# Optimization experiments

Measured on AMD Instinct MI355X. Metric: run time of the kernel, lower is better.

The kernel has to match this reference:

```python
import jax, jax.numpy as jnp
import numpy as np

N_LAYERS = 3
D = 32          # in = hidden = out channels (hardcoded in module)
N = 100_000     # nodes
E = 3_200_000   # edges (avg degree 32)
EPS = 1e-5
SLOPE = 0.01    # LeakyReLU default negative slope


def setup_inputs() -> dict:
    key = jax.random.key(0)
    ks = jax.random.split(key, 12)
    x = jax.random.normal(ks[0], (N, D), jnp.float32)
    edge_index = jax.random.randint(ks[1], (2, E), 0, N)
    edge_attr = jax.random.normal(ks[2], (E, 1), jnp.float32)  # unused by the conv
    s = 1.0 / np.sqrt(D)  # torch Linear default init range
    W = lambda k: jax.random.uniform(k, (N_LAYERS, D, D), jnp.float32, -s, s)
    b = lambda k: jax.random.uniform(k, (N_LAYERS, D), jnp.float32, -s, s)
    return dict(
        patch_embs=x, edge_index=edge_index, edge_attr=edge_attr,
        Wk=W(ks[3]), bk=b(ks[4]),   # lin_key   (applied to x_i / target)
        Wq=W(ks[5]), bq=b(ks[6]),   # lin_query (applied to x_j / source)
        Wv=W(ks[7]), bv=b(ks[8]),   # lin_value (applied to x_j / source)
        Ws=W(ks[9]), bs=b(ks[10]),  # lin_skip  (applied to x_i)
        gamma=jnp.ones((N_LAYERS, D), jnp.float32),
        beta=jnp.zeros((N_LAYERS, D), jnp.float32),
    )


def _res_gated_conv(x, Wk, bk, Wq, bq, Wv, bv, Ws, bs, src, dst):
    # Project per-node first (cheap), gather per-edge after.
    k = x @ Wk.T + bk   # [N,D] key   of target
    q = x @ Wq.T + bq   # [N,D] query of source
    v = x @ Wv.T + bv   # [N,D] value of source
    eta = jax.nn.sigmoid(k[dst] + q[src])          # [E,D] gate
    agg = jax.ops.segment_sum(eta * v[src], dst, num_segments=x.shape[0])
    return agg + (x @ Ws.T + bs)


def _batchnorm(x, g, b):
    mu = x.mean(axis=0)
    var = x.var(axis=0)  # biased, as in torch BN training forward
    return (x - mu) * jax.lax.rsqrt(var + EPS) * g + b


def _leaky(z):
    return jnp.where(z >= 0, z, SLOPE * z)


def reference(patch_embs, edge_index, edge_attr, Wk, bk, Wq, bq, Wv, bv, Ws, bs, gamma, beta):
    src, dst = edge_index[0], edge_index[1]
    h = patch_embs
    h = _batchnorm(_leaky(_res_gated_conv(h, Wk[0], bk[0], Wq[0], bq[0], Wv[0], bv[0], Ws[0], bs[0], src, dst)) + h, gamma[0], beta[0])
    h = _batchnorm(_leaky(_res_gated_conv(h, Wk[1], bk[1], Wq[1], bq[1], Wv[1], bv[1], Ws[1], bs[1], src, dst)) + h, gamma[1], beta[1])
    h = _batchnorm(_res_gated_conv(h, Wk[2], bk[2], Wq[2], bq[2], Wv[2], bv[2], Ws[2], bs[2], src, dst) + h, gamma[2], beta[2])
    return h
```

## Files before the change

### kernel.cpp

```cpp
#include <hip/hip_runtime.h>

#define DCH 32
#define EPSV 1e-5f
#define SLOPE 0.01f
#define SSTRIDE 16
#define BSH 7
#define BSZ 128
#define NBMAX 1024
#define CHUNK 8192
#define CAP 6144

__device__ __forceinline__ unsigned short f2bf(float x) {
    unsigned u = __float_as_uint(x);
    unsigned r = (u + 0x7FFFu + ((u >> 16) & 1u)) >> 16;
    return (unsigned short)r;
}
__device__ __forceinline__ float bf2f(unsigned short u) {
    return __uint_as_float(((unsigned)u) << 16);
}

__global__ __launch_bounds__(256) void k_bucket_hist(const int* __restrict__ dst,
                                                     int* __restrict__ bcnt, int E, int NB) {
    __shared__ int h[NBMAX];
    const int t = threadIdx.x;
    const int e0 = blockIdx.x * CHUNK;
    const int e1 = min(e0 + CHUNK, E);
    if (NB <= NBMAX) {
        for (int j = t; j < NB; j += 256) h[j] = 0;
        __syncthreads();
        for (int e = e0 + t; e < e1; e += 256) atomicAdd(&h[dst[e] >> BSH], 1);
        __syncthreads();
        for (int j = t; j < NB; j += 256) if (h[j]) atomicAdd(&bcnt[j], h[j]);
    } else {
        for (int e = e0 + t; e < e1; e += 256) atomicAdd(&bcnt[dst[e] >> BSH], 1);
    }
}

__global__ __launch_bounds__(1024) void k_scan(const int* __restrict__ deg, int* __restrict__ off, int N) {
    __shared__ int wsum[16];
    __shared__ int woff[16];
    __shared__ int ctot;
    __shared__ int carry;
    const int t = threadIdx.x;
    const int lane = t & 63;
    const int w = t >> 6;
    if (t == 0) carry = 0;
    __syncthreads();
    for (int base = 0; base < N; base += 1024) {
        const int i = base + t;
        const int v = (i < N) ? deg[i] : 0;
        int incl = v;
        #pragma unroll
        for (int d = 1; d < 64; d <<= 1) {
            int tmp = __shfl_up(incl, d);
            if (lane >= d) incl += tmp;
        }
        if (lane == 63) wsum[w] = incl;
        __syncthreads();
        if (t < 16) {
            const int a = wsum[t];
            int in = a;
            #pragma unroll
            for (int d = 1; d < 16; d <<= 1) {
                int tmp = __shfl_up(in, d);
                if (t >= d) in += tmp;
            }
            woff[t] = in - a;
            if (t == 15) ctot = in;
        }
        __syncthreads();
        if (i < N) off[i] = carry + woff[w] + incl - v;
        __syncthreads();
        if (t == 0) carry += ctot;
        __syncthreads();
    }
    if (t == 0) off[N] = carry;
}

__global__ __launch_bounds__(256) void k_bucket_scatter(const int* __restrict__ src, const int* __restrict__ dst,
                                                        const int* __restrict__ boff, int* __restrict__ cur,
                                                        unsigned int* __restrict__ pairs, int E, int NB) {
    const int t = threadIdx.x;
    const int e0 = blockIdx.x * CHUNK;
    const int e1 = min(e0 + CHUNK, E);
    if (NB <= NBMAX) {
        __shared__ int cnt[NBMAX];
        __shared__ int base[NBMAX];
        for (int j = t; j < NB; j += 256) { cnt[j] = 0; }
        __syncthreads();
        for (int e = e0 + t; e < e1; e += 256) atomicAdd(&cnt[dst[e] >> BSH], 1);
        __syncthreads();
        for (int j = t; j < NB; j += 256) {
            const int c = cnt[j];
            if (c) base[j] = atomicAdd(&cur[j], c);
            cnt[j] = 0;
        }
        __syncthreads();
        for (int e = e0 + t; e < e1; e += 256) {
            const int d = dst[e];
            const int bk = d >> BSH;
            const int r = atomicAdd(&cnt[bk], 1);
            pairs[boff[bk] + base[bk] + r] = ((unsigned)src[e] << BSH) | (unsigned)(d & (BSZ - 1));
        }
    } else {
        for (int e = e0 + t; e < e1; e += 256) {
            const int d = dst[e];
            const int bk = d >> BSH;
            const int r = atomicAdd(&cur[bk], 1);
            pairs[boff[bk] + r] = ((unsigned)src[e] << BSH) | (unsigned)(d & (BSZ - 1));
        }
    }
}

__global__ __launch_bounds__(256) void k_build_csr(const unsigned int* __restrict__ pairs,
                                                   const int* __restrict__ boff,
                                                   int* __restrict__ deg, int* __restrict__ off,
                                                   int* __restrict__ ssrc, int N) {
    __shared__ int cnt[BSZ];
    __shared__ int scn[BSZ];
    __shared__ int rnk[BSZ];
    __shared__ int stage[CAP];
    const int t = threadIdx.x;
    const int b = blockIdx.x;
    const int begin = boff[b], end = boff[b + 1];
    const int total = end - begin;
    if (t < BSZ) { cnt[t] = 0; rnk[t] = 0; }
    __syncthreads();
    for (int i = begin + t; i < end; i += 256) atomicAdd(&cnt[pairs[i] & (BSZ - 1)], 1);
    __syncthreads();
    if (t < BSZ) scn[t] = cnt[t];
    __syncthreads();
    #pragma unroll
    for (int s = 1; s < BSZ; s <<= 1) {
        int add = 0;
        if (t < BSZ && t >= s) add = scn[t - s];
        __syncthreads();
        if (t < BSZ) scn[t] += add;
        __syncthreads();
    }
    const int node0 = b << BSH;
    if (t < BSZ && node0 + t < N) {
        deg[node0 + t] = cnt[t];
        off[node0 + t] = begin + scn[t] - cnt[t];
    }
    if (total <= CAP) {
        for (int i = begin + t; i < end; i += 256) {
            const unsigned u = pairs[i];
            const int nl = u & (BSZ - 1);
            const int r = atomicAdd(&rnk[nl], 1);
            stage[scn[nl] - cnt[nl] + r] = (int)(u >> BSH);
        }
        __syncthreads();
        for (int i = t; i < total; i += 256) ssrc[begin + i] = stage[i];
    } else {
        for (int i = begin + t; i < end; i += 256) {
            const unsigned u = pairs[i];
            const int nl = u & (BSZ - 1);
            const int r = atomicAdd(&rnk[nl], 1);
            ssrc[begin + scn[nl] - cnt[nl] + r] = (int)(u >> BSH);
        }
    }
}

__global__ __launch_bounds__(256) void k_project(
    const float* __restrict__ xin,
    const float* __restrict__ statsPrev, const float* __restrict__ gPrev, const float* __restrict__ bPrev,
    const float* __restrict__ Wk, const float* __restrict__ bk,
    const float* __restrict__ Wq, const float* __restrict__ bq,
    const float* __restrict__ Wv, const float* __restrict__ bv,
    const float* __restrict__ Ws, const float* __restrict__ bs,
    float* __restrict__ kout, uint4* __restrict__ qvout,
    float* __restrict__ zout,
    int N, int do_bn, float invN)
{
    __shared__ float wk[DCH][DCH + 1], wq[DCH][DCH + 1], wv[DCH][DCH + 1], wsk[DCH][DCH + 1];
    __shared__ float xs[8][DCH];
    __shared__ unsigned short qvs[8][64];
    const int t = threadIdx.x;
    for (int i = t; i < DCH * DCH; i += 256) {
        const int c = i >> 5, d = i & 31;
        wk[c][d] = Wk[i];
        wq[c][d] = Wq[i];
        wv[c][d] = Wv[i];
        wsk[c][d] = Ws[i];
    }
    const int li = t >> 5;
    const int c  = t & 31;
    const int node = blockIdx.x * 8 + li;
    if (node < N) {
        float xv = xin[node * DCH + c];
        if (do_bn) {
            const float mn = statsPrev[c * SSTRIDE] * invN;
            const float var = statsPrev[1024 + c * SSTRIDE] * invN - mn * mn;
            const float sc = rsqrtf(var + EPSV) * gPrev[c];
            xv = (xv - mn) * sc + bPrev[c];
        }
        xs[li][c] = xv;
    }
    __syncthreads();
    float aK = 0.f, aQ = 0.f, aV = 0.f, aS = 0.f;
    if (node < N) {
        #pragma unroll
        for (int d = 0; d < DCH; ++d) {
            const float xv = xs[li][d];
            aK += xv * wk[c][d];
            aQ += xv * wq[c][d];
            aV += xv * wv[c][d];
            aS += xv * wsk[c][d];
        }
        const int o = node * DCH + c;
        kout[o] = aK + bk[c];
        zout[o] = aS + bs[c];
        const int g = c >> 2, j = c & 3;
        qvs[li][g * 8 + j]     = f2bf(aQ + bq[c]);
        qvs[li][g * 8 + 4 + j] = f2bf(aV + bv[c]);
    }
    __syncthreads();
    if (t < 64) {
        const int ln = t >> 3, g = t & 7;
        const int nd = blockIdx.x * 8 + ln;
        if (nd < N) qvout[nd * 8 + g] = ((const uint4*)qvs[ln])[g];
    }
}

__global__ __launch_bounds__(256) void k_edges_csr(
    const int* __restrict__ off, const int* __restrict__ deg, const int* __restrict__ ssrc,
    const float4* __restrict__ k4, const float4* __restrict__ qv4,
    const float4* __restrict__ zprev4,
    const float* __restrict__ statsPrev, const float* __restrict__ gPrev, const float* __restrict__ bPrev,
    float4* __restrict__ z4,
    float* __restrict__ statsCur, int N, int do_leaky, int do_bn, float invN)
{
    const int t = threadIdx.x;
    const int p = t & 7;
    const int lane = t & 63;
    const int w = t >> 6;
    const int groups = gridDim.x * 32;
    float scv[4] = {1.f, 1.f, 1.f, 1.f}, shv[4] = {0.f, 0.f, 0.f, 0.f};
    if (do_bn) {
        #pragma unroll
        for (int j = 0; j < 4; ++j) {
            const int c = p * 4 + j;
            const float mn = statsPrev[c * SSTRIDE] * invN;
            const float var = statsPrev[1024 + c * SSTRIDE] * invN - mn * mn;
            const float rs = rsqrtf(var + EPSV) * gPrev[c];
            scv[j] = rs;
            shv[j] = bPrev[c] - mn * rs;
        }
    }
    float s0 = 0.f, s1 = 0.f, s2 = 0.f, s3 = 0.f;
    float r0 = 0.f, r1 = 0.f, r2 = 0.f, r3 = 0.f;
    for (int n = blockIdx.x * 32 + (t >> 3); n < N; n += groups) {
        const int idx = n * 8 + p;
        const float4 kv = k4[idx];
        float ax = 0.f, ay = 0.f, az = 0.f, aw = 0.f;
        const int beg = off[n];
        const int end = beg + deg[n];
        for (int e = beg; e < end; ++e) {
            const int s = ssrc[e];
            union { float4 f; unsigned short us[8]; } U;
            U.f = qv4[(size_t)s * 8 + p];
            ax += bf2f(U.us[4]) / (1.f + __expf(-(kv.x + bf2f(U.us[0]))));
            ay += bf2f(U.us[5]) / (1.f + __expf(-(kv.y + bf2f(U.us[1]))));
            az += bf2f(U.us[6]) / (1.f + __expf(-(kv.z + bf2f(U.us[2]))));
            aw += bf2f(U.us[7]) / (1.f + __expf(-(kv.w + bf2f(U.us[3]))));
        }
        float4 z = z4[idx];
        z.x += ax; z.y += ay; z.z += az; z.w += aw;
        if (do_leaky) {
            z.x = z.x >= 0.f ? z.x : SLOPE * z.x;
            z.y = z.y >= 0.f ? z.y : SLOPE * z.y;
            z.z = z.z >= 0.f ? z.z : SLOPE * z.z;
            z.w = z.w >= 0.f ? z.w : SLOPE * z.w;
        }
        const float4 hz = zprev4[idx];
        z.x += hz.x * scv[0] + shv[0];
        z.y += hz.y * scv[1] + shv[1];
        z.z += hz.z * scv[2] + shv[2];
        z.w += hz.w * scv[3] + shv[3];
        z4[idx] = z;
        s0 += z.x; s1 += z.y; s2 += z.z; s3 += z.w;
        r0 += z.x * z.x; r1 += z.y * z.y; r2 += z.z * z.z; r3 += z.w * z.w;
    }
    #pragma unroll
    for (int d = 8; d < 64; d <<= 1) {
        s0 += __shfl_down(s0, d); s1 += __shfl_down(s1, d);
        s2 += __shfl_down(s2, d); s3 += __shfl_down(s3, d);
        r0 += __shfl_down(r0, d); r1 += __shfl_down(r1, d);
        r2 += __shfl_down(r2, d); r3 += __shfl_down(r3, d);
    }
    __shared__ float sm[4][DCH], sq[4][DCH];
    if (lane < 8) {
        sm[w][p * 4 + 0] = s0; sm[w][p * 4 + 1] = s1; sm[w][p * 4 + 2] = s2; sm[w][p * 4 + 3] = s3;
        sq[w][p * 4 + 0] = r0; sq[w][p * 4 + 1] = r1; sq[w][p * 4 + 2] = r2; sq[w][p * 4 + 3] = r3;
    }
    __syncthreads();
    if (t < DCH) {
        const float a = sm[0][t] + sm[1][t] + sm[2][t] + sm[3][t];
        const float b = sq[0][t] + sq[1][t] + sq[2][t] + sq[3][t];
        atomicAdd(&statsCur[t * SSTRIDE], a);
        atomicAdd(&statsCur[1024 + t * SSTRIDE], b);
    }
}

__global__ __launch_bounds__(256) void k_bn(
    const float* __restrict__ z, const float* __restrict__ stats,
    const float* __restrict__ gamma, const float* __restrict__ beta,
    float* __restrict__ out, int total, float invN)
{
    const int i = blockIdx.x * 256 + threadIdx.x;
    if (i >= total) return;
    const int c = i & 31;
    const float mean = stats[c * SSTRIDE] * invN;
    const float var  = stats[1024 + c * SSTRIDE] * invN - mean * mean;
    out[i] = (z[i] - mean) * rsqrtf(var + EPSV) * gamma[c] + beta[c];
}

extern "C" void kernel_launch(void* const* d_in, const int* in_sizes, int n_in,
                              void* d_out, int out_size, void* d_ws, size_t ws_size,
                              hipStream_t stream) {
    const float* x     = (const float*)d_in[0];
    const int*   ei    = (const int*)  d_in[1];
    const float* Wk    = (const float*)d_in[3];
    const float* bk    = (const float*)d_in[4];
    const float* Wq    = (const float*)d_in[5];
    const float* bq    = (const float*)d_in[6];
    const float* Wv    = (const float*)d_in[7];
    const float* bv    = (const float*)d_in[8];
    const float* Ws    = (const float*)d_in[9];
    const float* bs    = (const float*)d_in[10];
    const float* gamma = (const float*)d_in[11];
    const float* beta  = (const float*)d_in[12];

    const int N = in_sizes[0] / DCH;
    const int E = in_sizes[1] / 2;
    const int NB = (N + BSZ - 1) >> BSH;
    const int* src = ei;
    const int* dst = ei + E;

    float* ws     = (float*)d_ws;
    float* kbuf   = ws;
    unsigned short* qvbuf = (unsigned short*)(kbuf + (size_t)N * DCH);
    float* zA     = (float*)qvbuf + (size_t)N * DCH;
    float* zB     = zA + (size_t)N * DCH;
    float* statsA = zB + (size_t)N * DCH;
    float* statsB = statsA + 2048;
    int*   deg    = (int*)(statsB + 2048);
    int*   off    = deg + N;
    int*   bcnt   = off + N;
    int*   boff   = bcnt + NB;
    int*   cur    = boff + NB + 1;
    unsigned int* pairs = (unsigned int*)(cur + NB);
    int*   ssrc   = (int*)(pairs + E);

    const int total = N * DCH;
    const float invN = 1.f / (float)N;

    hipMemsetAsync(bcnt, 0, (size_t)NB * sizeof(int), stream);
    hipMemsetAsync(cur, 0, (size_t)NB * sizeof(int), stream);
    const int nchunk = (E + CHUNK - 1) / CHUNK;
    k_bucket_hist<<<nchunk, 256, 0, stream>>>(dst, bcnt, E, NB);
    k_scan<<<1, 1024, 0, stream>>>(bcnt, boff, NB);
    k_bucket_scatter<<<nchunk, 256, 0, stream>>>(src, dst, boff, cur, pairs, E, NB);
    k_build_csr<<<NB, 256, 0, stream>>>(pairs, boff, deg, off, ssrc, N);

    const float* zprev = x;
    const float* statsPrev = nullptr;
    for (int l = 0; l < 3; ++l) {
        const size_t wo = (size_t)l * DCH * DCH;
        const size_t bo = (size_t)l * DCH;
        float* zcur = (l & 1) ? zB : zA;
        float* statsCur = (l & 1) ? statsB : statsA;
        const float* gPrev = (l > 0) ? gamma + (size_t)(l - 1) * DCH : gamma;
        const float* bPrev = (l > 0) ? beta + (size_t)(l - 1) * DCH : beta;
        const int do_bn = (l > 0) ? 1 : 0;
        const float* sPrev = do_bn ? statsPrev : statsA;

        k_project<<<(N + 7) / 8, 256, 0, stream>>>(
            zprev, sPrev, gPrev, bPrev,
            Wk + wo, bk + bo, Wq + wo, bq + bo, Wv + wo, bv + bo, Ws + wo, bs + bo,
            kbuf, (uint4*)qvbuf, zcur, N, do_bn, invN);
        hipMemsetAsync(statsCur, 0, 2048 * sizeof(float), stream);
        k_edges_csr<<<2048, 256, 0, stream>>>(
            off, deg, ssrc, (const float4*)kbuf, (const float4*)qvbuf,
            (const float4*)zprev, sPrev, gPrev, bPrev,
            (float4*)zcur, statsCur, N, (l < 2) ? 1 : 0, do_bn, invN);

        statsPrev = statsCur;
        zprev = zcur;
    }
    k_bn<<<(total + 255) / 256, 256, 0, stream>>>(
        zA, statsA, gamma + 2 * DCH, beta + 2 * DCH, (float*)d_out, total, invN);
}
```

Measured before the change: 542.3 us.

## Fold -log2e into projections, use exp2/rcp sigmoid, fuse stats clear, one node per group

Pre-scales the key and query projections by -log2(e) so the per-edge sigmoid becomes exp2 plus a hardware reciprocal, with no negate or exp scaling. The bf16 unpacking now uses shifts and masks on uint4 words. The statistics buffer is zeroed inside the projection kernel instead of by a separate memset, which removes one launch per layer. The edge kernel switches from a 2048-block grid-stride loop to one node per 8-lane group over N/32 blocks, which raises the number of per-block atomic stat reductions and adds slight accuracy risk from the approximate rcp.

```diff
diff --git a/kernel.cpp b/kernel.cpp
--- a/kernel.cpp
+++ b/kernel.cpp
@@ -9,14 +9,27 @@
 #define NBMAX 1024
 #define CHUNK 8192
 #define CAP 6144
+#define LOG2E 1.4426950408889634f
+
+#if defined(__has_builtin)
+#  if __has_builtin(__builtin_amdgcn_exp2f)
+#    define EXP2F(x) __builtin_amdgcn_exp2f(x)
+#  endif
+#  if __has_builtin(__builtin_amdgcn_rcpf)
+#    define RCPF(x) __builtin_amdgcn_rcpf(x)
+#  endif
+#endif
+#ifndef EXP2F
+#  define EXP2F(x) exp2f(x)
+#endif
+#ifndef RCPF
+#  define RCPF(x) (1.0f / (x))
+#endif
 
 __device__ __forceinline__ unsigned short f2bf(float x) {
     unsigned u = __float_as_uint(x);
     unsigned r = (u + 0x7FFFu + ((u >> 16) & 1u)) >> 16;
     return (unsigned short)r;
-}
-__device__ __forceinline__ float bf2f(unsigned short u) {
-    return __uint_as_float(((unsigned)u) << 16);
 }
 
 __global__ __launch_bounds__(256) void k_bucket_hist(const int* __restrict__ dst,
@@ -170,13 +183,16 @@
     const float* __restrict__ Wv, const float* __restrict__ bv,
     const float* __restrict__ Ws, const float* __restrict__ bs,
     float* __restrict__ kout, uint4* __restrict__ qvout,
-    float* __restrict__ zout,
+    float* __restrict__ zout, float* __restrict__ statsCur,
     int N, int do_bn, float invN)
 {
     __shared__ float wk[DCH][DCH + 1], wq[DCH][DCH + 1], wv[DCH][DCH + 1], wsk[DCH][DCH + 1];
     __shared__ float xs[8][DCH];
     __shared__ unsigned short qvs[8][64];
     const int t = threadIdx.x;
+    if (blockIdx.x == 0) {
+        for (int i = t; i < 2048; i += 256) statsCur[i] = 0.f;
+    }
     for (int i = t; i < DCH * DCH; i += 256) {
         const int c = i >> 5, d = i & 31;
         wk[c][d] = Wk[i];
@@ -198,8 +214,8 @@
         xs[li][c] = xv;
     }
     __syncthreads();
-    float aK = 0.f, aQ = 0.f, aV = 0.f, aS = 0.f;
     if (node < N) {
+        float aK = 0.f, aQ = 0.f, aV = 0.f, aS = 0.f;
         #pragma unroll
         for (int d = 0; d < DCH; ++d) {
             const float xv = xs[li][d];
@@ -209,10 +225,10 @@
             aS += xv * wsk[c][d];
         }
         const int o = node * DCH + c;
-        kout[o] = aK + bk[c];
+        kout[o] = -LOG2E * (aK + bk[c]);
         zout[o] = aS + bs[c];
         const int g = c >> 2, j = c & 3;
-        qvs[li][g * 8 + j]     = f2bf(aQ + bq[c]);
+        qvs[li][g * 8 + j]     = f2bf(-LOG2E * (aQ + bq[c]));
         qvs[li][g * 8 + 4 + j] = f2bf(aV + bv[c]);
     }
     __syncthreads();
@@ -225,7 +241,7 @@
 
 __global__ __launch_bounds__(256) void k_edges_csr(
     const int* __restrict__ off, const int* __restrict__ deg, const int* __restrict__ ssrc,
-    const float4* __restrict__ k4, const float4* __restrict__ qv4,
+    const float4* __restrict__ kn4, const uint4* __restrict__ qv4,
     const float4* __restrict__ zprev4,
     const float* __restrict__ statsPrev, const float* __restrict__ gPrev, const float* __restrict__ bPrev,
     float4* __restrict__ z4,
@@ -235,7 +251,6 @@
     const int p = t & 7;
     const int lane = t & 63;
     const int w = t >> 6;
-    const int groups = gridDim.x * 32;
     float scv[4] = {1.f, 1.f, 1.f, 1.f}, shv[4] = {0.f, 0.f, 0.f, 0.f};
     if (do_bn) {
         #pragma unroll
@@ -250,20 +265,28 @@
     }
     float s0 = 0.f, s1 = 0.f, s2 = 0.f, s3 = 0.f;
     float r0 = 0.f, r1 = 0.f, r2 = 0.f, r3 = 0.f;
-    for (int n = blockIdx.x * 32 + (t >> 3); n < N; n += groups) {
+    const int n = blockIdx.x * 32 + (t >> 3);
+    if (n < N) {
         const int idx = n * 8 + p;
-        const float4 kv = k4[idx];
+        const float4 kn = kn4[idx];
         float ax = 0.f, ay = 0.f, az = 0.f, aw = 0.f;
         const int beg = off[n];
         const int end = beg + deg[n];
         for (int e = beg; e < end; ++e) {
             const int s = ssrc[e];
-            union { float4 f; unsigned short us[8]; } U;
-            U.f = qv4[(size_t)s * 8 + p];
-            ax += bf2f(U.us[4]) / (1.f + __expf(-(kv.x + bf2f(U.us[0]))));
-            ay += bf2f(U.us[5]) / (1.f + __expf(-(kv.y + bf2f(U.us[1]))));
-            az += bf2f(U.us[6]) / (1.f + __expf(-(kv.z + bf2f(U.us[2]))));
-            aw += bf2f(U.us[7]) / (1.f + __expf(-(kv.w + bf2f(U.us[3]))));
+            const uint4 u = qv4[(size_t)s * 8 + p];
+            const float q0 = __uint_as_float(u.x << 16);
+            const float q1 = __uint_as_float(u.x & 0xffff0000u);
+            const float q2 = __uint_as_float(u.y << 16);
+            const float q3 = __uint_as_float(u.y & 0xffff0000u);
+            const float v0 = __uint_as_float(u.z << 16);
+            const float v1 = __uint_as_float(u.z & 0xffff0000u);
+            const float v2 = __uint_as_float(u.w << 16);
+            const float v3 = __uint_as_float(u.w & 0xffff0000u);
+            ax = fmaf(v0, RCPF(1.f + EXP2F(kn.x + q0)), ax);
+            ay = fmaf(v1, RCPF(1.f + EXP2F(kn.y + q1)), ay);
+            az = fmaf(v2, RCPF(1.f + EXP2F(kn.z + q2)), az);
+            aw = fmaf(v3, RCPF(1.f + EXP2F(kn.w + q3)), aw);
         }
         float4 z = z4[idx];
         z.x += ax; z.y += ay; z.z += az; z.w += aw;
@@ -279,8 +302,8 @@
         z.z += hz.z * scv[2] + shv[2];
         z.w += hz.w * scv[3] + shv[3];
         z4[idx] = z;
-        s0 += z.x; s1 += z.y; s2 += z.z; s3 += z.w;
-        r0 += z.x * z.x; r1 += z.y * z.y; r2 += z.z * z.z; r3 += z.w * z.w;
+        s0 = z.x; s1 = z.y; s2 = z.z; s3 = z.w;
+        r0 = z.x * z.x; r1 = z.y * z.y; r2 = z.z * z.z; r3 = z.w * z.w;
     }
     #pragma unroll
     for (int d = 8; d < 64; d <<= 1) {
@@ -379,10 +402,9 @@
         k_project<<<(N + 7) / 8, 256, 0, stream>>>(
             zprev, sPrev, gPrev, bPrev,
             Wk + wo, bk + bo, Wq + wo, bq + bo, Wv + wo, bv + bo, Ws + wo, bs + bo,
-            kbuf, (uint4*)qvbuf, zcur, N, do_bn, invN);
-        hipMemsetAsync(statsCur, 0, 2048 * sizeof(float), stream);
-        k_edges_csr<<<2048, 256, 0, stream>>>(
-            off, deg, ssrc, (const float4*)kbuf, (const float4*)qvbuf,
+            kbuf, (uint4*)qvbuf, zcur, statsCur, N, do_bn, invN);
+        k_edges_csr<<<(N + 31) / 32, 256, 0, stream>>>(
+            off, deg, ssrc, (const float4*)kbuf, (const uint4*)qvbuf,
             (const float4*)zprev, sPrev, gPrev, bPrev,
             (float4*)zcur, statsCur, N, (l < 2) ? 1 : 0, do_bn, invN);
 
```

New measurement: 606.9 us. 1.12x slower.
